# Kernel tuning notes

Measured on AMD Instinct MI355X. Metric: run time of the kernel, lower is better.

The kernel has to match this reference:

```python
import jax, jax.numpy as jnp
import numpy as np

C = 1024        # channels
H = 16          # num_heads
D = C // H      # head dim = 64
WS = 512        # window_size
SHIFT = 256     # shift_sequence
MVD = 1024      # mv_dim
N = 16384       # total sparse tokens
EPS = 1e-6


def _ln32(x):
    # LayerNorm32: normalize in fp32, no affine (ln_affine=False), eps=1e-6
    x32 = x.astype(jnp.float32)
    m = jnp.mean(x32, axis=-1, keepdims=True)
    v = jnp.var(x32, axis=-1, keepdims=True)
    return ((x32 - m) * jax.lax.rsqrt(v + EPS)).astype(x.dtype)


def _shift_window_attn(h, qkv_w, qkv_b, proj_w, proj_b):
    # shift_sequence mode: roll serialized tokens, full attention within
    # contiguous windows of WS tokens, roll back.
    n = h.shape[0]
    hs = jnp.roll(h, -SHIFT, axis=0)
    qkv = hs @ qkv_w + qkv_b                      # [N, 3C]
    q, k, v = jnp.split(qkv, 3, axis=-1)
    nw = n // WS
    q = q.reshape(nw, WS, H, D)
    k = k.reshape(nw, WS, H, D)
    v = v.reshape(nw, WS, H, D)
    scale = 1.0 / np.sqrt(D)
    scores = jnp.einsum('wqhd,wkhd->whqk', q, k) * scale   # [nw,H,WS,WS]
    a = jax.nn.softmax(scores, axis=-1)
    o = jnp.einsum('whqk,wkhd->wqhd', a, v).reshape(n, C)
    o = jnp.roll(o, SHIFT, axis=0)
    return o @ proj_w + proj_b


def setup_inputs() -> dict:
    key = jax.random.key(0)
    ks = jax.random.split(key, 10)
    s = lambda fan_in: 1.0 / np.sqrt(fan_in)
    return {
        'x':         jax.random.normal(ks[0], (N, C), jnp.float32),
        'mv_normal': jax.random.normal(ks[1], (N, 4 * MVD), jnp.float32),
        'mv_color':  jax.random.normal(ks[2], (N, 4 * MVD), jnp.float32),
        'qkv_w':  jax.random.normal(ks[3], (C, 3 * C), jnp.float32) * s(C),
        'qkv_b':  jnp.zeros((3 * C,), jnp.float32),
        'proj_w': jax.random.normal(ks[4], (C, C), jnp.float32) * s(C),
        'proj_b': jnp.zeros((C,), jnp.float32),
        'mv_w1':  jax.random.normal(ks[5], (C + 8 * MVD, 4 * C), jnp.float32) * s(C + 8 * MVD),
        'mv_b1':  jnp.zeros((4 * C,), jnp.float32),
        'mv_w2':  jax.random.normal(ks[6], (4 * C, C), jnp.float32) * s(4 * C),
        'mv_b2':  jnp.zeros((C,), jnp.float32),
        'mlp_w1': jax.random.normal(ks[7], (C, 4 * C), jnp.float32) * s(C),
        'mlp_b1': jnp.zeros((4 * C,), jnp.float32),
        'mlp_w2': jax.random.normal(ks[8], (4 * C, C), jnp.float32) * s(4 * C),
        'mlp_b2': jnp.zeros((C,), jnp.float32),
    }


def reference(x, mv_normal, mv_color,
              qkv_w, qkv_b, proj_w, proj_b,
              mv_w1, mv_b1, mv_w2, mv_b2,
              mlp_w1, mlp_b1, mlp_w2, mlp_b2):
    # MSA branch: norm1 -> windowed sparse attention -> residual
    h = _shift_window_attn(_ln32(x), qkv_w, qkv_b, proj_w, proj_b)
    x = x + h
    # mv conditioning branch: norm3 -> concat(feats, mv_normal, mv_color) -> MLP -> residual
    h = _ln32(x)
    h = jnp.concatenate([h, mv_normal, mv_color], axis=1)   # [N, C + 8*MVD]
    h = jax.nn.gelu(h @ mv_w1 + mv_b1, approximate=True) @ mv_w2 + mv_b2
    x = x + h
    # FFN branch: norm2 -> SparseFeedForwardNet (Linear->GELU(tanh)->Linear) -> residual
    h = _ln32(x)
    h = jax.nn.gelu(h @ mlp_w1 + mlp_b1, approximate=True) @ mlp_w2 + mlp_b2
    return x + h
```

## Files before the change

kernel.cpp:

```cpp
#include <hip/hip_runtime.h>
#include <hip/hip_bf16.h>
#include <stdint.h>

#define N_TOK 16384
#define C_DIM 1024
#define NH    16
#define HD    64
#define WSZ   512
#define SHIFT_T 256

typedef __bf16 bf16x8 __attribute__((ext_vector_type(8)));
typedef float  f32x4  __attribute__((ext_vector_type(4)));
typedef unsigned short ushort_t;

__device__ __forceinline__ ushort_t f2bf(float f) {
    unsigned int x = __float_as_uint(f);
    unsigned int lsb = (x >> 16) & 1u;
    x += 0x7fffu + lsb;
    return (ushort_t)(x >> 16);
}

__device__ __forceinline__ float gelu_tanh(float v) {
    float v3 = v * v * v;
    float t = tanhf(0.7978845608028654f * (v + 0.044715f * v3));
    return 0.5f * v * (1.0f + t);
}

__global__ __launch_bounds__(256) void wt_transpose(const float* __restrict__ W,
                                                    ushort_t* __restrict__ WT,
                                                    int K, int M) {
    __shared__ float tile[64][65];
    const int k0 = blockIdx.y * 64;
    const int m0 = blockIdx.x * 64;
    const int tx = threadIdx.x & 63;
    const int ty = threadIdx.x >> 6;
#pragma unroll
    for (int p = 0; p < 16; p++) {
        tile[p * 4 + ty][tx] = W[(size_t)(k0 + p * 4 + ty) * M + m0 + tx];
    }
    __syncthreads();
#pragma unroll
    for (int p = 0; p < 16; p++) {
        WT[(size_t)(m0 + p * 4 + ty) * K + k0 + tx] = f2bf(tile[tx][p * 4 + ty]);
    }
}

__global__ __launch_bounds__(256) void ln_kernel(const float* __restrict__ src,
                                                 ushort_t* __restrict__ dst,
                                                 int dstStride, int rollShift) {
    const int row = blockIdx.x;
    const int tid = threadIdx.x;
    float4 v = reinterpret_cast<const float4*>(src + (size_t)row * C_DIM)[tid];
    float s = v.x + v.y + v.z + v.w;
    float q = v.x * v.x + v.y * v.y + v.z * v.z + v.w * v.w;
#pragma unroll
    for (int d = 1; d < 64; d <<= 1) {
        s += __shfl_xor(s, d);
        q += __shfl_xor(q, d);
    }
    __shared__ float red[8];
    if ((tid & 63) == 0) { red[(tid >> 6) * 2] = s; red[(tid >> 6) * 2 + 1] = q; }
    __syncthreads();
    s = red[0] + red[2] + red[4] + red[6];
    q = red[1] + red[3] + red[5] + red[7];
    const float mean = s * (1.0f / C_DIM);
    const float var  = q * (1.0f / C_DIM) - mean * mean;
    const float rs   = rsqrtf(var + 1e-6f);
    const int drow = (row - rollShift) & (N_TOK - 1);
    ushort4 o;
    o.x = f2bf((v.x - mean) * rs);
    o.y = f2bf((v.y - mean) * rs);
    o.z = f2bf((v.z - mean) * rs);
    o.w = f2bf((v.w - mean) * rs);
    reinterpret_cast<ushort4*>(dst + (size_t)drow * dstStride)[tid] = o;
}

__global__ __launch_bounds__(256) void cvt_cat(const float* __restrict__ mvn,
                                               const float* __restrict__ mvc,
                                               ushort_t* __restrict__ acat) {
    const int idx = blockIdx.x * 256 + threadIdx.x;
    const float4 v = reinterpret_cast<const float4*>(blockIdx.y ? mvc : mvn)[idx];
    const int row = idx >> 10;
    const int c4  = idx & 1023;
    ushort4 o;
    o.x = f2bf(v.x); o.y = f2bf(v.y); o.z = f2bf(v.z); o.w = f2bf(v.w);
    ushort_t* dst = acat + (size_t)row * 9216 + (blockIdx.y ? 5120 : 1024) + c4 * 4;
    *reinterpret_cast<ushort4*>(dst) = o;
}

__global__ __launch_bounds__(256) void gemm_bt(const ushort_t* __restrict__ A,
                                               const ushort_t* __restrict__ BT,
                                               const float* __restrict__ bias,
                                               const float* res,
                                               float* outF,
                                               ushort_t* __restrict__ outB,
                                               int K, int M, int mode, int rollA) {
    __shared__ ushort_t sA[3 * 128 * 32];
    __shared__ ushort_t sB[3 * 128 * 32];

    const int tid  = threadIdx.x;
    const int lane = tid & 63;
    const int wv   = tid >> 6;
    const int wrow = (wv >> 1) * 64;
    const int wcol = (wv & 1) * 64;
    const int rb = blockIdx.y * 128;
    const int cb = blockIdx.x * 128;
    const int quad = lane >> 4;
    const int l15  = lane & 15;

    const int sub = lane >> 2;
    const int kof = (lane & 3) * 8;
    int arow0 = rb + (wv * 2 + 0) * 16 + sub;
    int arow1 = rb + (wv * 2 + 1) * 16 + sub;
    if (rollA) {
        arow0 = (arow0 + N_TOK - SHIFT_T) & (N_TOK - 1);
        arow1 = (arow1 + N_TOK - SHIFT_T) & (N_TOK - 1);
    }
    const ushort_t* gA0 = A + (size_t)arow0 * K + kof;
    const ushort_t* gA1 = A + (size_t)arow1 * K + kof;
    const ushort_t* gB0 = BT + (size_t)(cb + (wv * 2 + 0) * 16 + sub) * K + kof;
    const ushort_t* gB1 = BT + (size_t)(cb + (wv * 2 + 1) * 16 + sub) * K + kof;
    const int c0 = (wv * 2 + 0) * 512;
    const int c1 = (wv * 2 + 1) * 512;

    auto stage = [&](int bufo, int kk) {
        __builtin_amdgcn_global_load_lds((const __attribute__((address_space(1))) void*)(gA0 + kk),
                                         (__attribute__((address_space(3))) void*)(sA + bufo + c0), 16, 0, 0);
        __builtin_amdgcn_global_load_lds((const __attribute__((address_space(1))) void*)(gA1 + kk),
                                         (__attribute__((address_space(3))) void*)(sA + bufo + c1), 16, 0, 0);
        __builtin_amdgcn_global_load_lds((const __attribute__((address_space(1))) void*)(gB0 + kk),
                                         (__attribute__((address_space(3))) void*)(sB + bufo + c0), 16, 0, 0);
        __builtin_amdgcn_global_load_lds((const __attribute__((address_space(1))) void*)(gB1 + kk),
                                         (__attribute__((address_space(3))) void*)(sB + bufo + c1), 16, 0, 0);
    };

    f32x4 acc[4][4];
    const f32x4 zero = {0.f, 0.f, 0.f, 0.f};
#pragma unroll
    for (int i = 0; i < 4; i++)
#pragma unroll
        for (int j = 0; j < 4; j++) acc[i][j] = zero;

    const int T = K >> 5;
    stage(0, 0);
    if (T > 1) stage(4096, 32);

    int curo = 0;
    for (int i = 0; i < T; i++) {
        if (i + 1 < T) __builtin_amdgcn_s_waitcnt(0x0F74);
        else           __builtin_amdgcn_s_waitcnt(0x0F70);
        asm volatile("s_barrier" ::: "memory");

        if (i + 2 < T) {
            int nxto = curo + 2 * 4096;
            if (nxto >= 3 * 4096) nxto -= 3 * 4096;
            stage(nxto, (i + 2) * 32);
        }

        const ushort_t* bA = sA + curo;
        const ushort_t* bB = sB + curo;
        bf16x8 av[4], bv[4];
#pragma unroll
        for (int mi = 0; mi < 4; mi++)
            av[mi] = *(const bf16x8*)(bA + (wrow + mi * 16 + l15) * 32 + quad * 8);
#pragma unroll
        for (int ni = 0; ni < 4; ni++)
            bv[ni] = *(const bf16x8*)(bB + (wcol + ni * 16 + l15) * 32 + quad * 8);
#pragma unroll
        for (int mi = 0; mi < 4; mi++)
#pragma unroll
            for (int ni = 0; ni < 4; ni++)
                acc[mi][ni] = __builtin_amdgcn_mfma_f32_16x16x32_bf16(av[mi], bv[ni], acc[mi][ni], 0, 0, 0);

        curo += 4096;
        if (curo >= 3 * 4096) curo = 0;
    }

#pragma unroll
    for (int ni = 0; ni < 4; ni++) {
        const int col = cb + wcol + ni * 16 + l15;
        const float bcol = bias[col];
#pragma unroll
        for (int mi = 0; mi < 4; mi++) {
#pragma unroll
            for (int r = 0; r < 4; r++) {
                const int row = rb + wrow + mi * 16 + quad * 4 + r;
                float v = acc[mi][ni][r] + bcol;
                if (mode == 0) {
                    outB[(size_t)row * M + col] = f2bf(v);
                } else if (mode == 1) {
                    outB[(size_t)row * M + col] = f2bf(gelu_tanh(v));
                } else {
                    outF[(size_t)row * M + col] = res[(size_t)row * M + col] + v;
                }
            }
        }
    }
}

__global__ __launch_bounds__(256) void attn_kernel(const ushort_t* __restrict__ qkv,
                                                   ushort_t* __restrict__ attn_o) {
    __shared__ ushort_t sQ[128 * 64];
    __shared__ ushort_t sK[64 * 64];
    __shared__ ushort_t sVT[64 * 64];
    __shared__ ushort_t sP[4][32 * 64];

    const int tid  = threadIdx.x;
    const int lane = tid & 63;
    const int wv   = tid >> 6;
    const int quad = lane >> 4;
    const int l15  = lane & 15;

    const int qc = blockIdx.x;
    const int h  = blockIdx.y;
    const int w  = blockIdx.z;
    const int qbase = w * WSZ + qc * 128;

    {
        const int r    = tid >> 1;
        const int half = (tid & 1) * 32;
        const ushort_t* src = qkv + (size_t)(qbase + r) * 3072 + h * 64 + half;
        const uint4* s4 = reinterpret_cast<const uint4*>(src);
        uint4* d4 = reinterpret_cast<uint4*>(sQ + r * 64 + half);
        d4[0] = s4[0]; d4[1] = s4[1]; d4[2] = s4[2]; d4[3] = s4[3];
    }

    f32x4 o[2][4];
    const f32x4 zero = {0.f, 0.f, 0.f, 0.f};
#pragma unroll
    for (int mi = 0; mi < 2; mi++)
#pragma unroll
        for (int ni = 0; ni < 4; ni++) o[mi][ni] = zero;
    float m_st[2][4], l_st[2][4];
#pragma unroll
    for (int mi = 0; mi < 2; mi++)
#pragma unroll
        for (int r = 0; r < 4; r++) { m_st[mi][r] = -3.0e38f; l_st[mi][r] = 0.f; }

    const int wq = wv * 32;

    for (int kt = 0; kt < 8; kt++) {
        __syncthreads();
        {
            const int key = tid >> 2;
            const int dq  = (tid & 3) * 16;
            const size_t rowb = (size_t)(w * WSZ + kt * 64 + key) * 3072;
            const uint4* sk4 = reinterpret_cast<const uint4*>(qkv + rowb + 1024 + h * 64 + dq);
            uint4* dk4 = reinterpret_cast<uint4*>(sK + key * 64 + dq);
            dk4[0] = sk4[0]; dk4[1] = sk4[1];
            const uint4* sv4 = reinterpret_cast<const uint4*>(qkv + rowb + 2048 + h * 64 + dq);
            uint4 a = sv4[0], b = sv4[1];
            const ushort_t* pa = reinterpret_cast<const ushort_t*>(&a);
            const ushort_t* pb = reinterpret_cast<const ushort_t*>(&b);
#pragma unroll
            for (int j = 0; j < 8; j++) {
                sVT[(dq + j) * 64 + key]     = pa[j];
                sVT[(dq + 8 + j) * 64 + key] = pb[j];
            }
        }
        __syncthreads();

        f32x4 s[2][4];
#pragma unroll
        for (int mi = 0; mi < 2; mi++)
#pragma unroll
            for (int ni = 0; ni < 4; ni++) s[mi][ni] = zero;
#pragma unroll
        for (int ks = 0; ks < 2; ks++) {
            bf16x8 aq[2], bk[4];
#pragma unroll
            for (int mi = 0; mi < 2; mi++)
                aq[mi] = *(const bf16x8*)(sQ + (wq + mi * 16 + l15) * 64 + ks * 32 + quad * 8);
#pragma unroll
            for (int ni = 0; ni < 4; ni++)
                bk[ni] = *(const bf16x8*)(sK + (ni * 16 + l15) * 64 + ks * 32 + quad * 8);
#pragma unroll
            for (int mi = 0; mi < 2; mi++)
#pragma unroll
                for (int ni = 0; ni < 4; ni++)
                    s[mi][ni] = __builtin_amdgcn_mfma_f32_16x16x32_bf16(aq[mi], bk[ni], s[mi][ni], 0, 0, 0);
        }
#pragma unroll
        for (int mi = 0; mi < 2; mi++)
#pragma unroll
            for (int ni = 0; ni < 4; ni++)
#pragma unroll
                for (int r = 0; r < 4; r++) s[mi][ni][r] *= 0.125f;

#pragma unroll
        for (int mi = 0; mi < 2; mi++) {
#pragma unroll
            for (int r = 0; r < 4; r++) {
                float rm = fmaxf(fmaxf(s[mi][0][r], s[mi][1][r]), fmaxf(s[mi][2][r], s[mi][3][r]));
#pragma unroll
                for (int d = 1; d < 16; d <<= 1) rm = fmaxf(rm, __shfl_xor(rm, d));
                const float mn = fmaxf(m_st[mi][r], rm);
                const float alpha = __expf(m_st[mi][r] - mn);
                float rsum = 0.f;
#pragma unroll
                for (int ni = 0; ni < 4; ni++) {
                    float p = __expf(s[mi][ni][r] - mn);
                    s[mi][ni][r] = p;
                    rsum += p;
                }
#pragma unroll
                for (int d = 1; d < 16; d <<= 1) rsum += __shfl_xor(rsum, d);
                l_st[mi][r] = l_st[mi][r] * alpha + rsum;
                m_st[mi][r] = mn;
#pragma unroll
                for (int ni = 0; ni < 4; ni++) o[mi][ni][r] *= alpha;
#pragma unroll
                for (int ni = 0; ni < 4; ni++)
                    sP[wv][(mi * 16 + quad * 4 + r) * 64 + ni * 16 + l15] = f2bf(s[mi][ni][r]);
            }
        }

#pragma unroll
        for (int ks = 0; ks < 2; ks++) {
            bf16x8 ap[2], bv2[4];
#pragma unroll
            for (int mi = 0; mi < 2; mi++)
                ap[mi] = *(const bf16x8*)(&sP[wv][(mi * 16 + l15) * 64 + ks * 32 + quad * 8]);
#pragma unroll
            for (int ni = 0; ni < 4; ni++)
                bv2[ni] = *(const bf16x8*)(sVT + (ni * 16 + l15) * 64 + ks * 32 + quad * 8);
#pragma unroll
            for (int mi = 0; mi < 2; mi++)
#pragma unroll
                for (int ni = 0; ni < 4; ni++)
                    o[mi][ni] = __builtin_amdgcn_mfma_f32_16x16x32_bf16(ap[mi], bv2[ni], o[mi][ni], 0, 0, 0);
        }
    }

#pragma unroll
    for (int mi = 0; mi < 2; mi++) {
#pragma unroll
        for (int r = 0; r < 4; r++) {
            const float inv = 1.0f / l_st[mi][r];
            const int row = qbase + wq + mi * 16 + quad * 4 + r;
#pragma unroll
            for (int ni = 0; ni < 4; ni++) {
                const int col = h * 64 + ni * 16 + l15;
                attn_o[(size_t)row * 1024 + col] = f2bf(o[mi][ni][r] * inv);
            }
        }
    }
}

extern "C" void kernel_launch(void* const* d_in, const int* in_sizes, int n_in,
                              void* d_out, int out_size, void* d_ws, size_t ws_size,
                              hipStream_t stream) {
    const float* x      = (const float*)d_in[0];
    const float* mv_n   = (const float*)d_in[1];
    const float* mv_c   = (const float*)d_in[2];
    const float* qkv_w  = (const float*)d_in[3];
    const float* qkv_b  = (const float*)d_in[4];
    const float* proj_w = (const float*)d_in[5];
    const float* proj_b = (const float*)d_in[6];
    const float* mv_w1  = (const float*)d_in[7];
    const float* mv_b1  = (const float*)d_in[8];
    const float* mv_w2  = (const float*)d_in[9];
    const float* mv_b2  = (const float*)d_in[10];
    const float* mlp_w1 = (const float*)d_in[11];
    const float* mlp_b1 = (const float*)d_in[12];
    const float* mlp_w2 = (const float*)d_in[13];
    const float* mlp_b2 = (const float*)d_in[14];
    float* out = (float*)d_out;

    char* ws = (char*)d_ws;
    size_t off = 0;
    auto alloc = [&](size_t bytes) {
        char* p = ws + off;
        off += (bytes + 255) & ~(size_t)255;
        return p;
    };
    ushort_t* w_qkv_t  = (ushort_t*)alloc((size_t)3072 * 1024 * 2);
    ushort_t* w_proj_t = (ushort_t*)alloc((size_t)1024 * 1024 * 2);
    ushort_t* w_mv1_t  = (ushort_t*)alloc((size_t)4096 * 9216 * 2);
    ushort_t* w_mv2_t  = (ushort_t*)alloc((size_t)1024 * 4096 * 2);
    ushort_t* w_mlp1_t = (ushort_t*)alloc((size_t)4096 * 1024 * 2);
    ushort_t* w_mlp2_t = (ushort_t*)alloc((size_t)1024 * 4096 * 2);
    ushort_t* lnbuf    = (ushort_t*)alloc((size_t)16384 * 1024 * 2);
    ushort_t* qkvmid   = (ushort_t*)alloc((size_t)16384 * 4096 * 2);
    ushort_t* attn_o   = (ushort_t*)alloc((size_t)16384 * 1024 * 2);
    float*    xacc     = (float*)alloc((size_t)16384 * 1024 * 4);
    ushort_t* acat     = (ushort_t*)alloc((size_t)16384 * 9216 * 2);

    wt_transpose<<<dim3(3072 / 64, 1024 / 64), 256, 0, stream>>>(qkv_w, w_qkv_t, 1024, 3072);
    wt_transpose<<<dim3(1024 / 64, 1024 / 64), 256, 0, stream>>>(proj_w, w_proj_t, 1024, 1024);
    wt_transpose<<<dim3(4096 / 64, 9216 / 64), 256, 0, stream>>>(mv_w1, w_mv1_t, 9216, 4096);
    wt_transpose<<<dim3(1024 / 64, 4096 / 64), 256, 0, stream>>>(mv_w2, w_mv2_t, 4096, 1024);
    wt_transpose<<<dim3(4096 / 64, 1024 / 64), 256, 0, stream>>>(mlp_w1, w_mlp1_t, 1024, 4096);
    wt_transpose<<<dim3(1024 / 64, 4096 / 64), 256, 0, stream>>>(mlp_w2, w_mlp2_t, 4096, 1024);

    ln_kernel<<<16384, 256, 0, stream>>>(x, lnbuf, 1024, SHIFT_T);
    gemm_bt<<<dim3(24, 128), 256, 0, stream>>>(lnbuf, w_qkv_t, qkv_b, nullptr, nullptr, qkvmid,
                                               1024, 3072, 0, 0);
    attn_kernel<<<dim3(4, 16, 32), 256, 0, stream>>>(qkvmid, attn_o);
    gemm_bt<<<dim3(8, 128), 256, 0, stream>>>(attn_o, w_proj_t, proj_b, x, xacc, nullptr,
                                              1024, 1024, 2, 1);

    ln_kernel<<<16384, 256, 0, stream>>>(xacc, acat, 9216, 0);
    cvt_cat<<<dim3(65536, 2), 256, 0, stream>>>(mv_n, mv_c, acat);
    gemm_bt<<<dim3(32, 128), 256, 0, stream>>>(acat, w_mv1_t, mv_b1, nullptr, nullptr, qkvmid,
                                               9216, 4096, 1, 0);
    gemm_bt<<<dim3(8, 128), 256, 0, stream>>>(qkvmid, w_mv2_t, mv_b2, xacc, xacc, nullptr,
                                              4096, 1024, 2, 0);

    ln_kernel<<<16384, 256, 0, stream>>>(xacc, lnbuf, 1024, 0);
    gemm_bt<<<dim3(32, 128), 256, 0, stream>>>(lnbuf, w_mlp1_t, mlp_b1, nullptr, nullptr, qkvmid,
                                               1024, 4096, 1, 0);
    gemm_bt<<<dim3(8, 128), 256, 0, stream>>>(qkvmid, w_mlp2_t, mlp_b2, xacc, out, nullptr,
                                              4096, 1024, 2, 0);
}
```

Measured before the change: 3.591 ms.

## Replace 128x128 GEMM with 256x256-tile 8-wave kernel using swizzled LDS and grid remap

```diff
diff --git a/kernel.cpp b/kernel.cpp
--- a/kernel.cpp
+++ b/kernel.cpp
@@ -88,103 +88,170 @@
     *reinterpret_cast<ushort4*>(dst) = o;
 }
 
-__global__ __launch_bounds__(256) void gemm_bt(const ushort_t* __restrict__ A,
-                                               const ushort_t* __restrict__ BT,
-                                               const float* __restrict__ bias,
-                                               const float* res,
-                                               float* outF,
-                                               ushort_t* __restrict__ outB,
-                                               int K, int M, int mode, int rollA) {
-    __shared__ ushort_t sA[3 * 128 * 32];
-    __shared__ ushort_t sB[3 * 128 * 32];
+#define TILE_E (256 * 64)
+
+__global__ __launch_bounds__(512, 2) void gemm256(const ushort_t* __restrict__ A,
+                                                  const ushort_t* __restrict__ BT,
+                                                  const float* __restrict__ bias,
+                                                  const float* res,
+                                                  float* outF,
+                                                  ushort_t* __restrict__ outB,
+                                                  int K, int M, int mode, int rollA) {
+    __shared__ ushort_t sA[2 * TILE_E];
+    __shared__ ushort_t sB[2 * TILE_E];
 
     const int tid  = threadIdx.x;
     const int lane = tid & 63;
     const int wv   = tid >> 6;
-    const int wrow = (wv >> 1) * 64;
-    const int wcol = (wv & 1) * 64;
-    const int rb = blockIdx.y * 128;
-    const int cb = blockIdx.x * 128;
+    const int wm   = wv >> 2;
+    const int wn   = wv & 3;
     const int quad = lane >> 4;
     const int l15  = lane & 15;
 
-    const int sub = lane >> 2;
-    const int kof = (lane & 3) * 8;
-    int arow0 = rb + (wv * 2 + 0) * 16 + sub;
-    int arow1 = rb + (wv * 2 + 1) * 16 + sub;
-    if (rollA) {
-        arow0 = (arow0 + N_TOK - SHIFT_T) & (N_TOK - 1);
-        arow1 = (arow1 + N_TOK - SHIFT_T) & (N_TOK - 1);
-    }
-    const ushort_t* gA0 = A + (size_t)arow0 * K + kof;
-    const ushort_t* gA1 = A + (size_t)arow1 * K + kof;
-    const ushort_t* gB0 = BT + (size_t)(cb + (wv * 2 + 0) * 16 + sub) * K + kof;
-    const ushort_t* gB1 = BT + (size_t)(cb + (wv * 2 + 1) * 16 + sub) * K + kof;
-    const int c0 = (wv * 2 + 0) * 512;
-    const int c1 = (wv * 2 + 1) * 512;
-
-    auto stage = [&](int bufo, int kk) {
-        __builtin_amdgcn_global_load_lds((const __attribute__((address_space(1))) void*)(gA0 + kk),
-                                         (__attribute__((address_space(3))) void*)(sA + bufo + c0), 16, 0, 0);
-        __builtin_amdgcn_global_load_lds((const __attribute__((address_space(1))) void*)(gA1 + kk),
-                                         (__attribute__((address_space(3))) void*)(sA + bufo + c1), 16, 0, 0);
-        __builtin_amdgcn_global_load_lds((const __attribute__((address_space(1))) void*)(gB0 + kk),
-                                         (__attribute__((address_space(3))) void*)(sB + bufo + c0), 16, 0, 0);
-        __builtin_amdgcn_global_load_lds((const __attribute__((address_space(1))) void*)(gB1 + kk),
-                                         (__attribute__((address_space(3))) void*)(sB + bufo + c1), 16, 0, 0);
-    };
-
-    f32x4 acc[4][4];
+    const int gx  = gridDim.x;
+    const int nwg = gx * gridDim.y;
+    const int lin = blockIdx.y * gx + blockIdx.x;
+    const int cpx = nwg >> 3;
+    const int swz = (lin & 7) * cpx + (lin >> 3);
+    const int rb  = (swz / gx) * 256;
+    const int cb  = (swz % gx) * 256;
+
+    const int sr     = lane >> 3;
+    const int schunk = (lane & 7) ^ sr;
+    const ushort_t* gAr[4];
+    const ushort_t* gBr[4];
+#pragma unroll
+    for (int l = 0; l < 4; l++) {
+        int rA = rb + l * 64 + wv * 8 + sr;
+        if (rollA) rA = (rA + N_TOK - SHIFT_T) & (N_TOK - 1);
+        gAr[l] = A + (size_t)rA * K + schunk * 8;
+        gBr[l] = BT + (size_t)(cb + l * 64 + wv * 8 + sr) * K + schunk * 8;
+    }
+    const int ldsStageOff = wv * 8 * 64;
+
+    auto stageA = [&](int buf, int t) {
+        const int kk = t << 6;
+#pragma unroll
+        for (int l = 0; l < 4; l++)
+            __builtin_amdgcn_global_load_lds(
+                (const __attribute__((address_space(1))) void*)(gAr[l] + kk),
+                (__attribute__((address_space(3))) void*)(sA + buf * TILE_E + l * 4096 + ldsStageOff),
+                16, 0, 0);
+    };
+    auto stageB = [&](int buf, int t) {
+        const int kk = t << 6;
+#pragma unroll
+        for (int l = 0; l < 4; l++)
+            __builtin_amdgcn_global_load_lds(
+                (const __attribute__((address_space(1))) void*)(gBr[l] + kk),
+                (__attribute__((address_space(3))) void*)(sB + buf * TILE_E + l * 4096 + ldsStageOff),
+                16, 0, 0);
+    };
+
+    auto rdA = [&](int buf, int mh, int kh, bf16x8* av) {
+        const ushort_t* base = sA + buf * TILE_E;
+#pragma unroll
+        for (int q = 0; q < 4; q++) {
+            const int row = wm * 128 + (mh * 4 + q) * 16 + l15;
+            const int e = row * 64 + (((kh * 4 + quad) ^ (l15 & 7)) << 3);
+            av[q] = *(const bf16x8*)(base + e);
+        }
+    };
+    auto rdB = [&](int buf, int kh, bf16x8* bv) {
+        const ushort_t* base = sB + buf * TILE_E;
+#pragma unroll
+        for (int n = 0; n < 4; n++) {
+            const int row = wn * 64 + n * 16 + l15;
+            const int e = row * 64 + (((kh * 4 + quad) ^ (l15 & 7)) << 3);
+            bv[n] = *(const bf16x8*)(base + e);
+        }
+    };
+
+    f32x4 acc[8][4];
     const f32x4 zero = {0.f, 0.f, 0.f, 0.f};
 #pragma unroll
-    for (int i = 0; i < 4; i++)
+    for (int i = 0; i < 8; i++)
 #pragma unroll
         for (int j = 0; j < 4; j++) acc[i][j] = zero;
 
-    const int T = K >> 5;
-    stage(0, 0);
-    if (T > 1) stage(4096, 32);
-
-    int curo = 0;
-    for (int i = 0; i < T; i++) {
-        if (i + 1 < T) __builtin_amdgcn_s_waitcnt(0x0F74);
-        else           __builtin_amdgcn_s_waitcnt(0x0F70);
-        asm volatile("s_barrier" ::: "memory");
-
-        if (i + 2 < T) {
-            int nxto = curo + 2 * 4096;
-            if (nxto >= 3 * 4096) nxto -= 3 * 4096;
-            stage(nxto, (i + 2) * 32);
-        }
-
-        const ushort_t* bA = sA + curo;
-        const ushort_t* bB = sB + curo;
-        bf16x8 av[4], bv[4];
-#pragma unroll
-        for (int mi = 0; mi < 4; mi++)
-            av[mi] = *(const bf16x8*)(bA + (wrow + mi * 16 + l15) * 32 + quad * 8);
-#pragma unroll
-        for (int ni = 0; ni < 4; ni++)
-            bv[ni] = *(const bf16x8*)(bB + (wcol + ni * 16 + l15) * 32 + quad * 8);
-#pragma unroll
-        for (int mi = 0; mi < 4; mi++)
-#pragma unroll
-            for (int ni = 0; ni < 4; ni++)
-                acc[mi][ni] = __builtin_amdgcn_mfma_f32_16x16x32_bf16(av[mi], bv[ni], acc[mi][ni], 0, 0, 0);
-
-        curo += 4096;
-        if (curo >= 3 * 4096) curo = 0;
-    }
+    auto mmac = [&](int mh, bf16x8* av, bf16x8* bv) {
+        __builtin_amdgcn_s_setprio(1);
+#pragma unroll
+        for (int q = 0; q < 4; q++)
+#pragma unroll
+            for (int n = 0; n < 4; n++)
+                acc[mh * 4 + q][n] =
+                    __builtin_amdgcn_mfma_f32_16x16x32_bf16(av[q], bv[n], acc[mh * 4 + q][n], 0, 0, 0);
+        __builtin_amdgcn_s_setprio(0);
+    };
+
+#define BAR()  asm volatile("s_barrier" ::: "memory")
+#define LGKM0() do { asm volatile("s_waitcnt lgkmcnt(0)" ::: "memory"); \
+                     __builtin_amdgcn_sched_barrier(0); } while (0)
+
+    const int T = K >> 6;
+
+    stageB(0, 0); stageA(0, 0); stageB(1, 1);
+    __builtin_amdgcn_s_waitcnt(0x0F74);
+    BAR();
+
+    bf16x8 av[4], bv[4];
+    const int nIt = T >> 1;
+    for (int i = 0; i < nIt; i++) {
+        const int t2 = 2 * i + 2;
+        const int t3 = 2 * i + 3;
+        rdA(0, 0, 0, av); rdB(0, 0, bv);
+        stageA(1, 2 * i + 1);
+        BAR(); LGKM0();
+        mmac(0, av, bv);
+        BAR();
+        rdA(0, 1, 0, av);
+        BAR(); LGKM0();
+        mmac(1, av, bv);
+        BAR();
+        rdA(0, 0, 1, av); rdB(0, 1, bv);
+        BAR(); LGKM0();
+        mmac(0, av, bv);
+        BAR();
+        rdA(0, 1, 1, av);
+        if (t2 < T) { stageB(0, t2); __builtin_amdgcn_s_waitcnt(0x0F74); }
+        else        { __builtin_amdgcn_s_waitcnt(0x0F70); }
+        BAR(); LGKM0();
+        mmac(1, av, bv);
+        BAR();
+        rdA(1, 0, 0, av); rdB(1, 0, bv);
+        if (t2 < T) stageA(0, t2);
+        BAR(); LGKM0();
+        mmac(0, av, bv);
+        BAR();
+        rdA(1, 1, 0, av);
+        BAR(); LGKM0();
+        mmac(1, av, bv);
+        BAR();
+        rdA(1, 0, 1, av); rdB(1, 1, bv);
+        BAR(); LGKM0();
+        mmac(0, av, bv);
+        BAR();
+        rdA(1, 1, 1, av);
+        if (t3 < T) { stageB(1, t3); __builtin_amdgcn_s_waitcnt(0x0F74); }
+        else        { __builtin_amdgcn_s_waitcnt(0x0F70); }
+        BAR(); LGKM0();
+        mmac(1, av, bv);
+        BAR();
+    }
+
+#undef BAR
+#undef LGKM0
 
 #pragma unroll
     for (int ni = 0; ni < 4; ni++) {
-        const int col = cb + wcol + ni * 16 + l15;
+        const int col = cb + wn * 64 + ni * 16 + l15;
         const float bcol = bias[col];
 #pragma unroll
-        for (int mi = 0; mi < 4; mi++) {
+        for (int mi = 0; mi < 8; mi++) {
 #pragma unroll
             for (int r = 0; r < 4; r++) {
-                const int row = rb + wrow + mi * 16 + quad * 4 + r;
+                const int row = rb + wm * 128 + mi * 16 + quad * 4 + r;
                 float v = acc[mi][ni][r] + bcol;
                 if (mode == 0) {
                     outB[(size_t)row * M + col] = f2bf(v);
@@ -394,22 +461,22 @@
     wt_transpose<<<dim3(1024 / 64, 4096 / 64), 256, 0, stream>>>(mlp_w2, w_mlp2_t, 4096, 1024);
 
     ln_kernel<<<16384, 256, 0, stream>>>(x, lnbuf, 1024, SHIFT_T);
-    gemm_bt<<<dim3(24, 128), 256, 0, stream>>>(lnbuf, w_qkv_t, qkv_b, nullptr, nullptr, qkvmid,
-                                               1024, 3072, 0, 0);
+    gemm256<<<dim3(12, 64), 512, 0, stream>>>(lnbuf, w_qkv_t, qkv_b, nullptr, nullptr, qkvmid,
+                                              1024, 3072, 0, 0);
     attn_kernel<<<dim3(4, 16, 32), 256, 0, stream>>>(qkvmid, attn_o);
-    gemm_bt<<<dim3(8, 128), 256, 0, stream>>>(attn_o, w_proj_t, proj_b, x, xacc, nullptr,
-                                              1024, 1024, 2, 1);
+    gemm256<<<dim3(4, 64), 512, 0, stream>>>(attn_o, w_proj_t, proj_b, x, xacc, nullptr,
+                                             1024, 1024, 2, 1);
 
     ln_kernel<<<16384, 256, 0, stream>>>(xacc, acat, 9216, 0);
     cvt_cat<<<dim3(65536, 2), 256, 0, stream>>>(mv_n, mv_c, acat);
-    gemm_bt<<<dim3(32, 128), 256, 0, stream>>>(acat, w_mv1_t, mv_b1, nullptr, nullptr, qkvmid,
-                                               9216, 4096, 1, 0);
-    gemm_bt<<<dim3(8, 128), 256, 0, stream>>>(qkvmid, w_mv2_t, mv_b2, xacc, xacc, nullptr,
-                                              4096, 1024, 2, 0);
+    gemm256<<<dim3(16, 64), 512, 0, stream>>>(acat, w_mv1_t, mv_b1, nullptr, nullptr, qkvmid,
+                                              9216, 4096, 1, 0);
+    gemm256<<<dim3(4, 64), 512, 0, stream>>>(qkvmid, w_mv2_t, mv_b2, xacc, xacc, nullptr,
+                                             4096, 1024, 2, 0);
 
     ln_kernel<<<16384, 256, 0, stream>>>(xacc, lnbuf, 1024, 0);
-    gemm_bt<<<dim3(32, 128), 256, 0, stream>>>(lnbuf, w_mlp1_t, mlp_b1, nullptr, nullptr, qkvmid,
-                                               1024, 4096, 1, 0);
-    gemm_bt<<<dim3(8, 128), 256, 0, stream>>>(qkvmid, w_mlp2_t, mlp_b2, xacc, out, nullptr,
-                                              4096, 1024, 2, 0);
-}
+    gemm256<<<dim3(16, 64), 512, 0, stream>>>(lnbuf, w_mlp1_t, mlp_b1, nullptr, nullptr, qkvmid,
+                                              1024, 4096, 1, 0);
+    gemm256<<<dim3(4, 64), 512, 0, stream>>>(qkvmid, w_mlp2_t, mlp_b2, xacc, out, nullptr,
+                                             4096, 1024, 2, 0);
+}
```

Result: faster. 3.083 ms (-14.2%).
